# Optimization experiments

Hardware: AMD Instinct MI355X
Metric: run time of the kernel (lower is better)

The kernel has to match this reference:

```python
import jax, jax.numpy as jnp
import numpy as np

KS = 7          # kernel_size
DIL = 1         # dilation
NUM_ITER = 10   # num_iterations
K2 = KS * KS
CENTER = K2 // 2  # self position removed from window


def _sliding_window(x):
    # x: [B, C, H, W] -> [B, C, K2-1, H, W], replicate-padded local windows
    pad = (KS - 1) * DIL // 2
    B, C, H, W = x.shape
    xp = jnp.pad(x, ((0, 0), (0, 0), (pad, pad), (pad, pad)), mode='edge')
    wins = [xp[:, :, i * DIL:i * DIL + H, j * DIL:j * DIL + W]
            for i in range(KS) for j in range(KS)]
    wins = wins[:CENTER] + wins[CENTER + 1:]  # remove_self=True
    return jnp.stack(wins, axis=2)


def _local_affinity(x):
    # x: [B, C, H, W] -> softmax-normalized affinity [B, 1, K2-1, H, W]
    q = x[:, :, None]                 # [B, C, 1, H, W]
    k = _sliding_window(x)            # [B, C, K2-1, H, W]
    std = jnp.std(k, axis=2, keepdims=True, ddof=1)  # torch .std is unbiased
    aff = -jnp.abs(k - q) / (1e-8 + 0.1 * std)
    aff = jnp.mean(aff, axis=1, keepdims=True)       # [B, 1, K2-1, H, W]
    return jax.nn.softmax(aff, axis=2)


def setup_inputs() -> dict:
    key = jax.random.key(0)
    k1, k2 = jax.random.split(key)
    feats = jax.random.normal(k1, (4, 3, 128, 128), dtype=jnp.float32)
    mask = jax.random.uniform(k2, (4, 21, 128, 128), dtype=jnp.float32)
    return {"feats": feats, "mask": mask}


def reference(feats, mask):
    aff = _local_affinity(feats)  # [B, 1, K2-1, H, W]

    def body(m, _):
        v = _sliding_window(m)            # [B, Cm, K2-1, H, W]
        return (v * aff).sum(axis=2), None

    mask, _ = jax.lax.scan(body, mask, None, length=NUM_ITER)
    return mask
```

## Files before the change

### kernel.cpp

```cpp
#include <hip/hip_runtime.h>

constexpr int B   = 4;
constexpr int CF  = 3;
constexpr int CM  = 21;
constexpr int H   = 128;
constexpr int W   = 128;
constexpr int KS  = 7;
constexpr int PAD = 3;
constexpr int CENTER = (KS * KS) / 2;
constexpr int NNB = KS * KS - 1;
constexpr int NUM_ITER = 10;

constexpr int TILE = 16;
constexpr int TH   = TILE + 2 * PAD;
constexpr int TS   = 24;
constexpr int HW   = H * W;

constexpr int IN   = TILE + 4 * PAD;
constexpr int IND  = 15;
constexpr int MD   = 22;
constexpr int MDD  = 13;
constexpr int CPB  = 7;
constexpr int NMID = MD * MD;

__device__ __forceinline__ unsigned short f2b(float v) {
    unsigned int x = __float_as_uint(v);
    x += 0x7fffu + ((x >> 16) & 1u);
    return (unsigned short)(x >> 16);
}
__device__ __forceinline__ float blo(unsigned int d) { return __uint_as_float(d << 16); }
__device__ __forceinline__ float bhi(unsigned int d) { return __uint_as_float(d & 0xffff0000u); }

__global__ __launch_bounds__(256) void aff_kernel(const float* __restrict__ feats,
                                                  float* __restrict__ aff) {
    __shared__ float tile[CF][TH][TS];
    const int tx = threadIdx.x, ty = threadIdx.y;
    const int bx = blockIdx.x * TILE, by = blockIdx.y * TILE;
    const int b  = blockIdx.z;
    const int tid = ty * TILE + tx;

    for (int c = 0; c < CF; ++c) {
        const float* src = feats + (size_t)(b * CF + c) * HW;
        for (int idx = tid; idx < TH * TH; idx += 256) {
            const int r  = idx / TH, cc = idx - r * TH;
            const int gh = min(max(by + r  - PAD, 0), H - 1);
            const int gw = min(max(bx + cc - PAD, 0), W - 1);
            tile[c][r][cc] = src[gh * W + gw];
        }
    }
    __syncthreads();

    float q[CF], inv[CF];
    #pragma unroll
    for (int c = 0; c < CF; ++c) {
        const float* tp = &tile[c][ty][tx];
        q[c] = tp[PAD * TS + PAD];
        float s = 0.f, s2 = 0.f;
        #pragma unroll
        for (int i = 0; i < KS; ++i)
            #pragma unroll
            for (int j = 0; j < KS; ++j) {
                if (i == PAD && j == PAD) continue;
                const float v = tp[i * TS + j];
                s += v; s2 += v * v;
            }
        const float mean = s * (1.0f / NNB);
        const float var  = fmaxf(s2 - (float)NNB * mean * mean, 0.f) * (1.0f / (NNB - 1));
        inv[c] = 1.0f / (1e-8f + 0.1f * sqrtf(var));
    }

    float a[NNB];
    float mx = -1e30f;
    #pragma unroll
    for (int i = 0; i < KS; ++i)
        #pragma unroll
        for (int j = 0; j < KS; ++j) {
            const int nn = i * KS + j;
            if (nn == CENTER) continue;
            const int n = (nn < CENTER) ? nn : nn - 1;
            float t = 0.f;
            #pragma unroll
            for (int c = 0; c < CF; ++c)
                t += fabsf(tile[c][ty + i][tx + j] - q[c]) * inv[c];
            a[n] = -t * (1.0f / CF);
            mx = fmaxf(mx, a[n]);
        }
    float ssum = 0.f;
    #pragma unroll
    for (int n = 0; n < NNB; ++n) { a[n] = __expf(a[n] - mx); ssum += a[n]; }
    const float rs = 1.0f / ssum;

    const int h = by + ty, w = bx + tx;
    #pragma unroll
    for (int n = 0; n < NNB; ++n)
        aff[(((size_t)b * NNB + n) * H + h) * W + w] = a[n] * rs;
}

__global__ __launch_bounds__(256, 3) void fuse2_kernel(const float* __restrict__ mi,
                                                       const float* __restrict__ aff,
                                                       float* __restrict__ mo) {
    __shared__ unsigned int in_u[CPB][IN][IND];
    __shared__ unsigned int mid_u[CPB][MD][MDD];

    const int tx = threadIdx.x, ty = threadIdx.y;
    const int tid = ty * TILE + tx;
    const int bx = blockIdx.x * TILE, by = blockIdx.y * TILE;
    const int zz = blockIdx.z;
    const int b  = zz / 3, g = zz % 3;
    const int c0 = g * CPB;

    const float* ab = aff + (size_t)b * NNB * HW;

    const int r1 = tid / MD, q1 = tid - r1 * MD;
    const int gh1 = min(max(by - PAD + r1, 0), H - 1);
    const int gw1 = min(max(bx - PAD + q1, 0), W - 1);

    float a[NNB];
    {
        const float* ap = ab + (size_t)gh1 * W + gw1;
        #pragma unroll
        for (int n = 0; n < NNB; ++n) a[n] = ap[(size_t)n * HW];
    }

    {
        const float* src = mi + (size_t)(b * CM + c0) * HW;
        for (int s = tid; s < IN * IN; s += 256) {
            const int rr = s / IN, qq = s - rr * IN;
            const int ih = min(max(by - 2 * PAD + rr, 0), H - 1);
            const int iw = min(max(bx - 2 * PAD + qq, 0), W - 1);
            const int go = ih * W + iw;
            #pragma unroll
            for (int c = 0; c < CPB; ++c)
                ((unsigned short*)&in_u[c][rr][0])[qq] = f2b(src[c * HW + go]);
        }
    }
    __syncthreads();

    {
        const int ar = gh1 - by + PAD;
        const int ac = gw1 - bx + PAD;
        const int k0 = (ac & ~1) >> 1;
        const bool par = (ac & 1);
        #pragma unroll
        for (int c = 0; c < CPB; ++c) {
            float s = 0.f;
            #pragma unroll
            for (int i = 0; i < KS; ++i) {
                const unsigned int* rp = &in_u[c][ar + i][0];
                const unsigned int d0 = rp[k0], d1 = rp[k0+1], d2 = rp[k0+2], d3 = rp[k0+3];
                const float e0=blo(d0), e1=bhi(d0), e2=blo(d1), e3=bhi(d1),
                            e4=blo(d2), e5=bhi(d2), e6=blo(d3), e7=bhi(d3);
                const float w0 = par?e1:e0, w1 = par?e2:e1, w2 = par?e3:e2,
                            w3 = par?e4:e3, w4 = par?e5:e4, w5 = par?e6:e5, w6 = par?e7:e6;
                const float wv[7] = { w0, w1, w2, w3, w4, w5, w6 };
                #pragma unroll
                for (int j = 0; j < KS; ++j) {
                    const int nn = i * KS + j;
                    if (nn == CENTER) continue;
                    const int n = (nn < CENTER) ? nn : nn - 1;
                    s += a[n] * wv[j];
                }
            }
            ((unsigned short*)&mid_u[c][r1][0])[q1] = f2b(s);
        }
    }

    {
        const int m2 = (tid + 256 < NMID) ? tid + 256 : NMID - 1;
        const int r2 = m2 / MD, q2 = m2 - r2 * MD;
        const int gh2 = min(max(by - PAD + r2, 0), H - 1);
        const int gw2 = min(max(bx - PAD + q2, 0), W - 1);
        {
            const float* ap = ab + (size_t)gh2 * W + gw2;
            #pragma unroll
            for (int n = 0; n < NNB; ++n) a[n] = ap[(size_t)n * HW];
        }
        const int ar = gh2 - by + PAD;
        const int ac = gw2 - bx + PAD;
        const int k0 = (ac & ~1) >> 1;
        const bool par = (ac & 1);
        const bool wr = (tid + 256 < NMID);
        #pragma unroll
        for (int c = 0; c < CPB; ++c) {
            float s = 0.f;
            #pragma unroll
            for (int i = 0; i < KS; ++i) {
                const unsigned int* rp = &in_u[c][ar + i][0];
                const unsigned int d0 = rp[k0], d1 = rp[k0+1], d2 = rp[k0+2], d3 = rp[k0+3];
                const float e0=blo(d0), e1=bhi(d0), e2=blo(d1), e3=bhi(d1),
                            e4=blo(d2), e5=bhi(d2), e6=blo(d3), e7=bhi(d3);
                const float w0 = par?e1:e0, w1 = par?e2:e1, w2 = par?e3:e2,
                            w3 = par?e4:e3, w4 = par?e5:e4, w5 = par?e6:e5, w6 = par?e7:e6;
                const float wv[7] = { w0, w1, w2, w3, w4, w5, w6 };
                #pragma unroll
                for (int j = 0; j < KS; ++j) {
                    const int nn = i * KS + j;
                    if (nn == CENTER) continue;
                    const int n = (nn < CENTER) ? nn : nn - 1;
                    s += a[n] * wv[j];
                }
            }
            if (wr) ((unsigned short*)&mid_u[c][r2][0])[q2] = f2b(s);
        }
    }
    __syncthreads();

    {
        const int oh = by + ty, ow = bx + tx;
        {
            const float* ap = ab + (size_t)oh * W + ow;
            #pragma unroll
            for (int n = 0; n < NNB; ++n) a[n] = ap[(size_t)n * HW];
        }
        const int k0 = (tx & ~1) >> 1;
        const bool par = (tx & 1);
        float* dp = mo + (size_t)(b * CM + c0) * HW + (size_t)oh * W + ow;
        #pragma unroll
        for (int c = 0; c < CPB; ++c) {
            float s = 0.f;
            #pragma unroll
            for (int i = 0; i < KS; ++i) {
                const unsigned int* rp = &mid_u[c][ty + i][0];
                const unsigned int d0 = rp[k0], d1 = rp[k0+1], d2 = rp[k0+2], d3 = rp[k0+3];
                const float e0=blo(d0), e1=bhi(d0), e2=blo(d1), e3=bhi(d1),
                            e4=blo(d2), e5=bhi(d2), e6=blo(d3), e7=bhi(d3);
                const float w0 = par?e1:e0, w1 = par?e2:e1, w2 = par?e3:e2,
                            w3 = par?e4:e3, w4 = par?e5:e4, w5 = par?e6:e5, w6 = par?e7:e6;
                const float wv[7] = { w0, w1, w2, w3, w4, w5, w6 };
                #pragma unroll
                for (int j = 0; j < KS; ++j) {
                    const int nn = i * KS + j;
                    if (nn == CENTER) continue;
                    const int n = (nn < CENTER) ? nn : nn - 1;
                    s += a[n] * wv[j];
                }
            }
            dp[(size_t)c * HW] = s;
        }
    }
}

extern "C" void kernel_launch(void* const* d_in, const int* in_sizes, int n_in,
                              void* d_out, int out_size, void* d_ws, size_t ws_size,
                              hipStream_t stream) {
    const float* feats = (const float*)d_in[0];
    const float* mask  = (const float*)d_in[1];
    float* out = (float*)d_out;

    float* aff  = (float*)d_ws;
    float* buf0 = aff  + (size_t)B * NNB * HW;
    float* buf1 = buf0 + (size_t)B * CM  * HW;

    aff_kernel<<<dim3(W / TILE, H / TILE, B), dim3(TILE, TILE), 0, stream>>>(feats, aff);

    dim3 grid(W / TILE, H / TILE, B * 3);
    dim3 blk(TILE, TILE);
    fuse2_kernel<<<grid, blk, 0, stream>>>(mask, aff, buf0);
    fuse2_kernel<<<grid, blk, 0, stream>>>(buf0, aff, buf1);
    fuse2_kernel<<<grid, blk, 0, stream>>>(buf1, aff, buf0);
    fuse2_kernel<<<grid, blk, 0, stream>>>(buf0, aff, buf1);
    fuse2_kernel<<<grid, blk, 0, stream>>>(buf1, aff, out);
}
```

Before: 144.0 us.

## Store shifted-by-one bf16 shared copies and reassign mid-tile work to halo/interior

Keeps two bf16 copies of each shared-memory tile, one shifted by a single element, so every thread reads an aligned 4-word run and the per-element parity selects are gone. Mid-tile work is split differently: 228 threads compute the halo ring of the intermediate, then all 256 threads compute the 16x16 interior using affinities they later reuse in the final pass, which removes one affinity reload and the idle remainder threads. The cost is double the shared-memory writes and footprint, which may affect occupancy at 3 blocks per CU.

```diff
diff --git a/kernel.cpp b/kernel.cpp
--- a/kernel.cpp
+++ b/kernel.cpp
@@ -19,9 +19,10 @@
 constexpr int IN   = TILE + 4 * PAD;
 constexpr int IND  = 15;
 constexpr int MD   = 22;
-constexpr int MDD  = 13;
+constexpr int MDD  = 12;
 constexpr int CPB  = 7;
-constexpr int NMID = MD * MD;
+constexpr int INP  = CPB * IN * IND;
+constexpr int MDP  = CPB * MD * MDD;
 
 __device__ __forceinline__ unsigned short f2b(float v) {
     unsigned int x = __float_as_uint(v);
@@ -99,8 +100,8 @@
 __global__ __launch_bounds__(256, 3) void fuse2_kernel(const float* __restrict__ mi,
                                                        const float* __restrict__ aff,
                                                        float* __restrict__ mo) {
-    __shared__ unsigned int in_u[CPB][IN][IND];
-    __shared__ unsigned int mid_u[CPB][MD][MDD];
+    __shared__ unsigned int in_u[2 * INP];
+    __shared__ unsigned int md_u[2 * MDP];
 
     const int tx = threadIdx.x, ty = threadIdx.y;
     const int tid = ty * TILE + tx;
@@ -111,13 +112,18 @@
 
     const float* ab = aff + (size_t)b * NNB * HW;
 
-    const int r1 = tid / MD, q1 = tid - r1 * MD;
-    const int gh1 = min(max(by - PAD + r1, 0), H - 1);
-    const int gw1 = min(max(bx - PAD + q1, 0), W - 1);
+    const int t2 = min(tid, 227);
+    int rr_, qq_;
+    if (t2 < 66)       { rr_ = t2 / MD;                    qq_ = t2 - rr_ * MD; }
+    else if (t2 < 132) { const int s = t2 - 66;  rr_ = 19 + s / MD; qq_ = s % MD; }
+    else               { const int s = t2 - 132; rr_ = 3 + s / 6;
+                         const int u = s % 6;    qq_ = (u < 3) ? u : 16 + u; }
+    const int gh_r = min(max(by - PAD + rr_, 0), H - 1);
+    const int gw_r = min(max(bx - PAD + qq_, 0), W - 1);
 
     float a[NNB];
     {
-        const float* ap = ab + (size_t)gh1 * W + gw1;
+        const float* ap = ab + (size_t)gh_r * W + gw_r;
         #pragma unroll
         for (int n = 0; n < NNB; ++n) a[n] = ap[(size_t)n * HW];
     }
@@ -130,29 +136,32 @@
             const int iw = min(max(bx - 2 * PAD + qq, 0), W - 1);
             const int go = ih * W + iw;
             #pragma unroll
-            for (int c = 0; c < CPB; ++c)
-                ((unsigned short*)&in_u[c][rr][0])[qq] = f2b(src[c * HW + go]);
+            for (int c = 0; c < CPB; ++c) {
+                const unsigned short v = f2b(src[c * HW + go]);
+                unsigned short* rowA = (unsigned short*)&in_u[(c * IN + rr) * IND];
+                unsigned short* rowB = (unsigned short*)&in_u[INP + (c * IN + rr) * IND];
+                rowA[qq] = v;
+                if (qq >= 1) rowB[qq - 1] = v;
+            }
         }
     }
     __syncthreads();
 
     {
-        const int ar = gh1 - by + PAD;
-        const int ac = gw1 - bx + PAD;
-        const int k0 = (ac & ~1) >> 1;
-        const bool par = (ac & 1);
+        const int ar = gh_r - by + PAD;
+        const int ac = gw_r - bx + PAD;
+        const int psel = (ac & 1) ? INP : 0;
+        const int k0 = ac >> 1;
+        const bool wr = (tid < 228);
         #pragma unroll
         for (int c = 0; c < CPB; ++c) {
             float s = 0.f;
             #pragma unroll
             for (int i = 0; i < KS; ++i) {
-                const unsigned int* rp = &in_u[c][ar + i][0];
-                const unsigned int d0 = rp[k0], d1 = rp[k0+1], d2 = rp[k0+2], d3 = rp[k0+3];
-                const float e0=blo(d0), e1=bhi(d0), e2=blo(d1), e3=bhi(d1),
-                            e4=blo(d2), e5=bhi(d2), e6=blo(d3), e7=bhi(d3);
-                const float w0 = par?e1:e0, w1 = par?e2:e1, w2 = par?e3:e2,
-                            w3 = par?e4:e3, w4 = par?e5:e4, w5 = par?e6:e5, w6 = par?e7:e6;
-                const float wv[7] = { w0, w1, w2, w3, w4, w5, w6 };
+                const unsigned int* rp = &in_u[psel + (c * IN + ar + i) * IND + k0];
+                const unsigned int d0 = rp[0], d1 = rp[1], d2 = rp[2], d3 = rp[3];
+                const float wv[7] = { blo(d0), bhi(d0), blo(d1), bhi(d1),
+                                      blo(d2), bhi(d2), blo(d3) };
                 #pragma unroll
                 for (int j = 0; j < KS; ++j) {
                     const int nn = i * KS + j;
@@ -161,37 +170,34 @@
                     s += a[n] * wv[j];
                 }
             }
-            ((unsigned short*)&mid_u[c][r1][0])[q1] = f2b(s);
-        }
-    }
-
-    {
-        const int m2 = (tid + 256 < NMID) ? tid + 256 : NMID - 1;
-        const int r2 = m2 / MD, q2 = m2 - r2 * MD;
-        const int gh2 = min(max(by - PAD + r2, 0), H - 1);
-        const int gw2 = min(max(bx - PAD + q2, 0), W - 1);
-        {
-            const float* ap = ab + (size_t)gh2 * W + gw2;
-            #pragma unroll
-            for (int n = 0; n < NNB; ++n) a[n] = ap[(size_t)n * HW];
-        }
-        const int ar = gh2 - by + PAD;
-        const int ac = gw2 - bx + PAD;
-        const int k0 = (ac & ~1) >> 1;
-        const bool par = (ac & 1);
-        const bool wr = (tid + 256 < NMID);
+            if (wr) {
+                const unsigned short v = f2b(s);
+                ((unsigned short*)&md_u[(c * MD + rr_) * MDD])[qq_] = v;
+                if (qq_ >= 1)
+                    ((unsigned short*)&md_u[MDP + (c * MD + rr_) * MDD])[qq_ - 1] = v;
+            }
+        }
+    }
+
+    {
+        const float* ap = ab + (size_t)(by + ty) * W + (bx + tx);
+        #pragma unroll
+        for (int n = 0; n < NNB; ++n) a[n] = ap[(size_t)n * HW];
+    }
+    {
+        const int ar = ty + PAD, ac = tx + PAD;
+        const int psel = (ac & 1) ? INP : 0;
+        const int k0 = ac >> 1;
+        const int mq = tx + PAD;
         #pragma unroll
         for (int c = 0; c < CPB; ++c) {
             float s = 0.f;
             #pragma unroll
             for (int i = 0; i < KS; ++i) {
-                const unsigned int* rp = &in_u[c][ar + i][0];
-                const unsigned int d0 = rp[k0], d1 = rp[k0+1], d2 = rp[k0+2], d3 = rp[k0+3];
-                const float e0=blo(d0), e1=bhi(d0), e2=blo(d1), e3=bhi(d1),
-                            e4=blo(d2), e5=bhi(d2), e6=blo(d3), e7=bhi(d3);
-                const float w0 = par?e1:e0, w1 = par?e2:e1, w2 = par?e3:e2,
-                            w3 = par?e4:e3, w4 = par?e5:e4, w5 = par?e6:e5, w6 = par?e7:e6;
-                const float wv[7] = { w0, w1, w2, w3, w4, w5, w6 };
+                const unsigned int* rp = &in_u[psel + (c * IN + ar + i) * IND + k0];
+                const unsigned int d0 = rp[0], d1 = rp[1], d2 = rp[2], d3 = rp[3];
+                const float wv[7] = { blo(d0), bhi(d0), blo(d1), bhi(d1),
+                                      blo(d2), bhi(d2), blo(d3) };
                 #pragma unroll
                 for (int j = 0; j < KS; ++j) {
                     const int nn = i * KS + j;
@@ -200,33 +206,26 @@
                     s += a[n] * wv[j];
                 }
             }
-            if (wr) ((unsigned short*)&mid_u[c][r2][0])[q2] = f2b(s);
+            const unsigned short v = f2b(s);
+            ((unsigned short*)&md_u[(c * MD + ty + PAD) * MDD])[mq] = v;
+            ((unsigned short*)&md_u[MDP + (c * MD + ty + PAD) * MDD])[mq - 1] = v;
         }
     }
     __syncthreads();
 
     {
-        const int oh = by + ty, ow = bx + tx;
-        {
-            const float* ap = ab + (size_t)oh * W + ow;
-            #pragma unroll
-            for (int n = 0; n < NNB; ++n) a[n] = ap[(size_t)n * HW];
-        }
-        const int k0 = (tx & ~1) >> 1;
-        const bool par = (tx & 1);
-        float* dp = mo + (size_t)(b * CM + c0) * HW + (size_t)oh * W + ow;
+        const int psel = (tx & 1) ? MDP : 0;
+        const int k0 = tx >> 1;
+        float* dp = mo + (size_t)(b * CM + c0) * HW + (size_t)(by + ty) * W + (bx + tx);
         #pragma unroll
         for (int c = 0; c < CPB; ++c) {
             float s = 0.f;
             #pragma unroll
             for (int i = 0; i < KS; ++i) {
-                const unsigned int* rp = &mid_u[c][ty + i][0];
-                const unsigned int d0 = rp[k0], d1 = rp[k0+1], d2 = rp[k0+2], d3 = rp[k0+3];
-                const float e0=blo(d0), e1=bhi(d0), e2=blo(d1), e3=bhi(d1),
-                            e4=blo(d2), e5=bhi(d2), e6=blo(d3), e7=bhi(d3);
-                const float w0 = par?e1:e0, w1 = par?e2:e1, w2 = par?e3:e2,
-                            w3 = par?e4:e3, w4 = par?e5:e4, w5 = par?e6:e5, w6 = par?e7:e6;
-                const float wv[7] = { w0, w1, w2, w3, w4, w5, w6 };
+                const unsigned int* rp = &md_u[psel + (c * MD + ty + i) * MDD + k0];
+                const unsigned int d0 = rp[0], d1 = rp[1], d2 = rp[2], d3 = rp[3];
+                const float wv[7] = { blo(d0), bhi(d0), blo(d1), bhi(d1),
+                                      blo(d2), bhi(d2), blo(d3) };
                 #pragma unroll
                 for (int j = 0; j < KS; ++j) {
                     const int nn = i * KS + j;
```

Measured after the change: 160.6 us. +11.5%, slower.
